# Kernel optimization log

Measured on AMD Instinct MI355X. Metric: run time of the kernel, lower is better.

Reference implementation:

```python
import jax, jax.numpy as jnp
import numpy as np

N_NODES = 50000
N_EDGES = 1000000
IN_DIM, HID_DIM, OUT_DIM = 128, 64, 16


def setup_inputs() -> dict:
    key = jax.random.key(0)
    k1, k2, k3, k4 = jax.random.split(key, 4)
    x = jax.random.normal(k1, (N_NODES, IN_DIM), dtype=jnp.float32)
    edge_index = jax.random.randint(k2, (2, N_EDGES), 0, N_NODES, dtype=jnp.int64)
    # Glorot-style scaling for weights, zero bias (PyG GCNConv default init style)
    W1 = jax.random.normal(k3, (IN_DIM, HID_DIM), dtype=jnp.float32) * (1.0 / np.sqrt(IN_DIM))
    b1 = jnp.zeros((HID_DIM,), dtype=jnp.float32)
    W2 = jax.random.normal(k4, (HID_DIM, OUT_DIM), dtype=jnp.float32) * (1.0 / np.sqrt(HID_DIM))
    b2 = jnp.zeros((OUT_DIM,), dtype=jnp.float32)
    return {"x": x, "edge_index": edge_index, "W1": W1, "b1": b1, "W2": W2, "b2": b2}


def gcn_conv(x, src, dst, W, b, num_nodes):
    """PyG GCNConv: add self loops, symmetric deg^{-1/2} normalization,
    linear transform, gather-scale-scatter aggregation, bias."""
    # degree includes self loops (src/dst already augmented by caller)
    deg = jax.ops.segment_sum(jnp.ones_like(dst, dtype=x.dtype), dst, num_segments=num_nodes)
    dinv = jnp.where(deg > 0, deg ** -0.5, 0.0)
    norm = dinv[src] * dinv[dst]            # [E']
    h = x @ W                                # [N, F_out] transform before aggregation
    msg = h[src] * norm[:, None]             # gather + scale
    out = jax.ops.segment_sum(msg, dst, num_segments=num_nodes)  # scatter-add
    return out + b


def reference(x, edge_index, W1, b1, W2, b2):
    n = x.shape[0]
    loops = jnp.arange(n, dtype=edge_index.dtype)
    src = jnp.concatenate([edge_index[0], loops])
    dst = jnp.concatenate([edge_index[1], loops])
    h = gcn_conv(x, src, dst, W1, b1, n)
    h = jax.nn.relu(h)
    out = gcn_conv(h, src, dst, W2, b2, n)
    return out
```

## Files before the change

### kernel.cpp

```cpp
#include <hip/hip_runtime.h>

#define IN_DIM 128
#define HID_DIM 64
#define OUT_DIM 16

#define SSHIFT 7
#define SMASK 127
#define CHUNK 4096
#define CBLK 256
#define KPT (CHUNK / CBLK)
#define CAP 4096

static __device__ __forceinline__ unsigned short f2bf(float f) {
    unsigned u = __float_as_uint(f);
    unsigned r = u + 0x7fffu + ((u >> 16) & 1u);
    return (unsigned short)(r >> 16);
}
static __device__ __forceinline__ unsigned packbf2(float a, float b) {
    return (unsigned)f2bf(a) | ((unsigned)f2bf(b) << 16);
}
static __device__ __forceinline__ float bflo(unsigned v) { return __uint_as_float(v << 16); }
static __device__ __forceinline__ float bfhi(unsigned v) { return __uint_as_float(v & 0xffff0000u); }

__global__ __launch_bounds__(CBLK) void passC2(const int* __restrict__ src,
                                               const int* __restrict__ dst,
                                               int* __restrict__ gcnt,
                                               int* __restrict__ eb,
                                               int E, int NS) {
    __shared__ int cnt[512];
    __shared__ int bofs[512];
    int t = threadIdx.x;
    for (int s = t; s < NS; s += CBLK) cnt[s] = 0;
    __syncthreads();
    int base = blockIdx.x * CHUNK;
    int dreg[KPT];
    #pragma unroll
    for (int k = 0; k < KPT; ++k) {
        int i = base + k * CBLK + t;
        int d = -1;
        if (i < E) { d = dst[i]; atomicAdd(&cnt[d >> SSHIFT], 1); }
        dreg[k] = d;
    }
    __syncthreads();
    for (int s = t; s < NS; s += CBLK) {
        int c = cnt[s];
        bofs[s] = c ? atomicAdd(&gcnt[s], c) : 0;
        cnt[s] = 0;
    }
    __syncthreads();
    #pragma unroll
    for (int k = 0; k < KPT; ++k) {
        int i = base + k * CBLK + t;
        if (i < E) {
            int d = dreg[k];
            int s = d >> SSHIFT;
            int off = atomicAdd(&cnt[s], 1);
            eb[(size_t)s * CAP + bofs[s] + off] = src[i] | ((d & SMASK) << 17);
        }
    }
}

__global__ __launch_bounds__(256) void passD(const int* __restrict__ eb,
                                             const int* __restrict__ tot,
                                             int* __restrict__ csr_src,
                                             int* __restrict__ row_ptr,
                                             float* __restrict__ dinv,
                                             int N, int E, int NS) {
    __shared__ int red[256];
    __shared__ int deg[128], incl[128], cur[128];
    int s = blockIdx.x, t = threadIdx.x;
    if (t < 128) deg[t] = 0;
    int part = 0;
    for (int k = t; k < s; k += 256) part += tot[k];
    red[t] = part;
    __syncthreads();
    for (int off = 128; off >= 1; off >>= 1) {
        if (t < off) red[t] += red[t + off];
        __syncthreads();
    }
    int b0 = red[0];
    int cnt = tot[s];
    const size_t sbase = (size_t)s * CAP;
    for (int k = t; k < cnt; k += 256) atomicAdd(&deg[eb[sbase + k] >> 17], 1);
    __syncthreads();
    if (t < 128) incl[t] = deg[t];
    __syncthreads();
    for (int off = 1; off < 128; off <<= 1) {
        int tmp = 0;
        if (t < 128 && t >= off) tmp = incl[t - off];
        __syncthreads();
        if (t < 128) incl[t] += tmp;
        __syncthreads();
    }
    if (t < 128) {
        int loff = incl[t] - deg[t];
        cur[t] = b0 + loff;
        int n = (s << SSHIFT) + t;
        if (n < N) {
            row_ptr[n] = b0 + loff;
            dinv[n] = rsqrtf((float)(deg[t] + 1));
        }
    }
    if (s == NS - 1 && t == 0) row_ptr[N] = E;
    __syncthreads();
    for (int k = t; k < cnt; k += 256) {
        int v = eb[sbase + k];
        int dl = v >> 17;
        int p = atomicAdd(&cur[dl], 1);
        csr_src[p] = v & 0x1FFFF;
    }
}

__global__ __launch_bounds__(256) void gemm1_kernel(const float* __restrict__ x,
                                                    const float* __restrict__ W1,
                                                    const float* __restrict__ dinv,
                                                    unsigned* __restrict__ h1u, int N) {
    __shared__ __align__(16) float sW[IN_DIM * HID_DIM];
    __shared__ __align__(16) float sx[16 * IN_DIM];
    int t = threadIdx.x;
    int node0 = blockIdx.x * 16;

    const float4* W4  = (const float4*)W1;
    float4*       sW4 = (float4*)sW;
    for (int i = t; i < (IN_DIM * HID_DIM) / 4; i += 256) sW4[i] = W4[i];

    const float4* x4  = (const float4*)x;
    float4*       sx4 = (float4*)sx;
    for (int i = t; i < (16 * IN_DIM) / 4; i += 256) {
        int r = i >> 5, c = i & 31;
        int n = node0 + r; if (n >= N) n = 0;
        sx4[(r << 5) + c] = x4[(size_t)n * 32 + c];
    }
    __syncthreads();

    int ln = t >> 4, jj = t & 15;
    int n = node0 + ln;
    float4 acc = {0.f, 0.f, 0.f, 0.f};
    const float* xr = sx + ln * IN_DIM;
    #pragma unroll 4
    for (int k = 0; k < IN_DIM; ++k) {
        float  xk = xr[k];
        float4 wv = ((const float4*)(sW + k * HID_DIM))[jj];
        acc.x += xk * wv.x; acc.y += xk * wv.y; acc.z += xk * wv.z; acc.w += xk * wv.w;
    }
    if (n <= N) {
        float dn = (n < N) ? dinv[n] : 0.f;
        uint2 pv;
        pv.x = packbf2(acc.x * dn, acc.y * dn);
        pv.y = packbf2(acc.z * dn, acc.w * dn);
        ((uint2*)(h1u + (size_t)n * 32))[jj] = pv;
    }
}

__global__ __launch_bounds__(256) void agg1_kernel(const unsigned* __restrict__ h1u,
                                                   const int* __restrict__ row_ptr,
                                                   const int* __restrict__ csr_src,
                                                   const float* __restrict__ dinv,
                                                   const float* __restrict__ b1,
                                                   const float* __restrict__ W2,
                                                   unsigned* __restrict__ h2u, int N) {
    __shared__ __align__(16) float sW[OUT_DIM * 68];
    int t = threadIdx.x;
    for (int i = t; i < HID_DIM * OUT_DIM; i += 256) {
        int k = i >> 4, j = i & 15;
        sW[j * 68 + k] = W2[i];
    }
    __syncthreads();

    int lane = t & 63;
    int h  = lane >> 5;
    int l  = lane & 31;
    int es = l >> 3;
    int dg = l & 7;
    int n = blockIdx.x * 8 + ((t >> 6) << 1) + h;
    if (n > N) return;
    if (n == N) {
        if (l < 4) { uint2 z; z.x = 0u; z.y = 0u; ((uint2*)h2u)[(size_t)N * 4 + l] = z; }
        return;
    }

    int e0 = row_ptr[n], e1 = row_ptr[n + 1];
    const uint4* rb = (const uint4*)h1u;
    int sb = h << 5;

    float a0 = 0.f, a1 = 0.f, a2 = 0.f, a3 = 0.f,
          a4 = 0.f, a5 = 0.f, a6 = 0.f, a7 = 0.f;

    for (int base = e0 - 1; base < e1; base += 32) {
        int idx = base + l;
        int sld = N;
        if (idx == e0 - 1) sld = n;
        else if (idx < e1) sld = csr_src[idx];
        int lim = e1 - base;
        if (lim > 32) lim = 32;
        int nr = (lim + 3) >> 2;
        nr = (nr + 1) & ~1;
        for (int r = 0; r < nr; r += 2) {
            int sA = __shfl(sld, sb + ((r + 0) << 2) + es);
            int sB = __shfl(sld, sb + ((r + 1) << 2) + es);
            uint4 vA = rb[(size_t)sA * 8 + dg];
            uint4 vB = rb[(size_t)sB * 8 + dg];
            a0 += bflo(vA.x) + bflo(vB.x);
            a1 += bfhi(vA.x) + bfhi(vB.x);
            a2 += bflo(vA.y) + bflo(vB.y);
            a3 += bfhi(vA.y) + bfhi(vB.y);
            a4 += bflo(vA.z) + bflo(vB.z);
            a5 += bfhi(vA.z) + bfhi(vB.z);
            a6 += bflo(vA.w) + bflo(vB.w);
            a7 += bfhi(vA.w) + bfhi(vB.w);
        }
    }
    #pragma unroll
    for (int m = 8; m <= 16; m <<= 1) {
        a0 += __shfl_xor(a0, m); a1 += __shfl_xor(a1, m);
        a2 += __shfl_xor(a2, m); a3 += __shfl_xor(a3, m);
        a4 += __shfl_xor(a4, m); a5 += __shfl_xor(a5, m);
        a6 += __shfl_xor(a6, m); a7 += __shfl_xor(a7, m);
    }

    float dn = dinv[n];
    float4 bA = ((const float4*)b1)[2 * dg];
    float4 bB = ((const float4*)b1)[2 * dg + 1];
    float r0 = fmaxf(fmaf(dn, a0, bA.x), 0.f);
    float r1 = fmaxf(fmaf(dn, a1, bA.y), 0.f);
    float r2 = fmaxf(fmaf(dn, a2, bA.z), 0.f);
    float r3 = fmaxf(fmaf(dn, a3, bA.w), 0.f);
    float r4 = fmaxf(fmaf(dn, a4, bB.x), 0.f);
    float r5 = fmaxf(fmaf(dn, a5, bB.y), 0.f);
    float r6 = fmaxf(fmaf(dn, a6, bB.z), 0.f);
    float r7 = fmaxf(fmaf(dn, a7, bB.w), 0.f);

    const float* wb = sW + ((es << 2) * 68) + (dg << 3);
    float4 wA, wB2;
    wA = *(const float4*)(wb);        wB2 = *(const float4*)(wb + 4);
    float p0 = r0*wA.x + r1*wA.y + r2*wA.z + r3*wA.w + r4*wB2.x + r5*wB2.y + r6*wB2.z + r7*wB2.w;
    wA = *(const float4*)(wb + 68);   wB2 = *(const float4*)(wb + 72);
    float p1 = r0*wA.x + r1*wA.y + r2*wA.z + r3*wA.w + r4*wB2.x + r5*wB2.y + r6*wB2.z + r7*wB2.w;
    wA = *(const float4*)(wb + 136);  wB2 = *(const float4*)(wb + 140);
    float p2 = r0*wA.x + r1*wA.y + r2*wA.z + r3*wA.w + r4*wB2.x + r5*wB2.y + r6*wB2.z + r7*wB2.w;
    wA = *(const float4*)(wb + 204);  wB2 = *(const float4*)(wb + 208);
    float p3 = r0*wA.x + r1*wA.y + r2*wA.z + r3*wA.w + r4*wB2.x + r5*wB2.y + r6*wB2.z + r7*wB2.w;

    #pragma unroll
    for (int m = 1; m <= 4; m <<= 1) {
        p0 += __shfl_xor(p0, m); p1 += __shfl_xor(p1, m);
        p2 += __shfl_xor(p2, m); p3 += __shfl_xor(p3, m);
    }
    if (dg == 0) {
        uint2 pv;
        pv.x = packbf2(p0 * dn, p1 * dn);
        pv.y = packbf2(p2 * dn, p3 * dn);
        ((uint2*)h2u)[(size_t)n * 4 + es] = pv;
    }
}

__global__ __launch_bounds__(256) void agg2_kernel(const unsigned* __restrict__ h2u,
                                                   const int* __restrict__ row_ptr,
                                                   const int* __restrict__ csr_src,
                                                   const float* __restrict__ dinv,
                                                   const float* __restrict__ b2,
                                                   float* __restrict__ out, int N) {
    int t = threadIdx.x;
    int lane = t & 63;
    int h  = lane >> 4;
    int l  = lane & 15;
    int es = l >> 2;
    int dg = l & 3;
    int n = blockIdx.x * 16 + ((t >> 6) << 2) + h;
    if (n >= N) return;

    int e0 = row_ptr[n], e1 = row_ptr[n + 1];
    const uint2* rb = (const uint2*)h2u;
    int sb = h << 4;

    float a0 = 0.f, a1 = 0.f, a2 = 0.f, a3 = 0.f;

    for (int base = e0 - 1; base < e1; base += 16) {
        int idx = base + l;
        int sld = N;
        if (idx == e0 - 1) sld = n;
        else if (idx < e1) sld = csr_src[idx];
        int lim = e1 - base;
        if (lim > 16) lim = 16;
        int nr = (lim + 3) >> 2;
        nr = (nr + 1) & ~1;
        for (int r = 0; r < nr; r += 2) {
            int sA = __shfl(sld, sb + ((r + 0) << 2) + es);
            int sB = __shfl(sld, sb + ((r + 1) << 2) + es);
            uint2 vA = rb[(size_t)sA * 4 + dg];
            uint2 vB = rb[(size_t)sB * 4 + dg];
            a0 += bflo(vA.x) + bflo(vB.x);
            a1 += bfhi(vA.x) + bfhi(vB.x);
            a2 += bflo(vA.y) + bflo(vB.y);
            a3 += bfhi(vA.y) + bfhi(vB.y);
        }
    }
    #pragma unroll
    for (int m = 4; m <= 8; m <<= 1) {
        a0 += __shfl_xor(a0, m); a1 += __shfl_xor(a1, m);
        a2 += __shfl_xor(a2, m); a3 += __shfl_xor(a3, m);
    }
    if (es == 0) {
        float dn = dinv[n];
        float4 bb = ((const float4*)b2)[dg];
        float4 r;
        r.x = fmaf(dn, a0, bb.x);
        r.y = fmaf(dn, a1, bb.y);
        r.z = fmaf(dn, a2, bb.z);
        r.w = fmaf(dn, a3, bb.w);
        ((float4*)out)[(size_t)n * 4 + dg] = r;
    }
}

extern "C" void kernel_launch(void* const* d_in, const int* in_sizes, int n_in,
                              void* d_out, int out_size, void* d_ws, size_t ws_size,
                              hipStream_t stream) {
    const float* x  = (const float*)d_in[0];
    const int*   ei = (const int*)d_in[1];
    const float* W1 = (const float*)d_in[2];
    const float* b1 = (const float*)d_in[3];
    const float* W2 = (const float*)d_in[4];
    const float* b2 = (const float*)d_in[5];
    float* out = (float*)d_out;

    const int N = in_sizes[0] / IN_DIM;
    const int E = in_sizes[1] / 2;
    const int* src = ei;
    const int* dst = ei + E;

    const int NS  = (N + SMASK) >> SSHIFT;
    const int NSP = NS + 1;
    const int BC  = (E + CHUNK - 1) / CHUNK;

    char* w = (char*)d_ws;
    auto alloc = [&](size_t bytes) -> void* {
        void* p = (void*)w;
        w += (bytes + 255) & ~(size_t)255;
        return p;
    };
    int*      gcnt    = (int*)     alloc((size_t)NSP * 4);
    int*      eb      = (int*)     alloc((size_t)NS * CAP * 4);
    int*      csr_src = (int*)     alloc((size_t)E * 4);
    int*      row_ptr = (int*)     alloc((size_t)(N + 1) * 4);
    float*    dinv    = (float*)   alloc((size_t)N * 4);
    unsigned* h1u     = (unsigned*)alloc((size_t)(N + 1) * 32 * 4);
    unsigned* h2u     = (unsigned*)alloc((size_t)(N + 1) * 8 * 4);

    const int GB  = (N + 16) / 16;
    const int AB1 = (N + 8) / 8;
    const int AB2 = (N + 15) / 16;

    hipMemsetAsync(gcnt, 0, (size_t)NSP * 4, stream);
    passC2<<<BC, CBLK, 0, stream>>>(src, dst, gcnt, eb, E, NS);
    passD <<<NS, 256,  0, stream>>>(eb, gcnt, csr_src, row_ptr, dinv, N, E, NS);

    gemm1_kernel<<<GB, 256, 0, stream>>>(x, W1, dinv, h1u, N);
    agg1_kernel<<<AB1, 256, 0, stream>>>(h1u, row_ptr, csr_src, dinv, b1, W2, h2u, N);
    agg2_kernel<<<AB2, 256, 0, stream>>>(h2u, row_ptr, csr_src, dinv, b2, out, N);
}
```

Before: 165.8 us.

## Fuse edge bucketing with GEMM1 and apply source normalization during aggregation

The bucketing pass and the first dense transform now run as one launch, with block ranges split between the two jobs. This removes the dependency of the GEMM on dinv, so the two can overlap and one launch is saved. The source-side dinv scaling moves into agg1 as an extra per-edge gather of dinv[src] feeding FMAs. The GEMM also reads W1 straight from global memory instead of staging it in shared memory. The risk is the extra per-edge load in agg1, plus cached global reads of W1 in every GEMM block.

```diff
diff --git a/kernel.cpp b/kernel.cpp
--- a/kernel.cpp
+++ b/kernel.cpp
@@ -22,40 +22,81 @@
 static __device__ __forceinline__ float bflo(unsigned v) { return __uint_as_float(v << 16); }
 static __device__ __forceinline__ float bfhi(unsigned v) { return __uint_as_float(v & 0xffff0000u); }
 
-__global__ __launch_bounds__(CBLK) void passC2(const int* __restrict__ src,
-                                               const int* __restrict__ dst,
-                                               int* __restrict__ gcnt,
-                                               int* __restrict__ eb,
-                                               int E, int NS) {
-    __shared__ int cnt[512];
-    __shared__ int bofs[512];
-    int t = threadIdx.x;
-    for (int s = t; s < NS; s += CBLK) cnt[s] = 0;
-    __syncthreads();
-    int base = blockIdx.x * CHUNK;
-    int dreg[KPT];
-    #pragma unroll
-    for (int k = 0; k < KPT; ++k) {
-        int i = base + k * CBLK + t;
-        int d = -1;
-        if (i < E) { d = dst[i]; atomicAdd(&cnt[d >> SSHIFT], 1); }
-        dreg[k] = d;
-    }
-    __syncthreads();
-    for (int s = t; s < NS; s += CBLK) {
-        int c = cnt[s];
-        bofs[s] = c ? atomicAdd(&gcnt[s], c) : 0;
-        cnt[s] = 0;
-    }
-    __syncthreads();
-    #pragma unroll
-    for (int k = 0; k < KPT; ++k) {
-        int i = base + k * CBLK + t;
-        if (i < E) {
-            int d = dreg[k];
-            int s = d >> SSHIFT;
-            int off = atomicAdd(&cnt[s], 1);
-            eb[(size_t)s * CAP + bofs[s] + off] = src[i] | ((d & SMASK) << 17);
+__global__ __launch_bounds__(256) void build_kernel(const float* __restrict__ x,
+                                                    const int* __restrict__ ei,
+                                                    const float* __restrict__ W1,
+                                                    int* __restrict__ gcnt,
+                                                    int* __restrict__ eb,
+                                                    unsigned* __restrict__ h1u,
+                                                    int N, int E, int NS, int BC) {
+    __shared__ __align__(16) int smem[2048];
+    const int t = threadIdx.x;
+    const int b = blockIdx.x;
+
+    if (b < BC) {
+        const int* src = ei;
+        const int* dst = ei + E;
+        int* cnt  = smem;
+        int* bofs = smem + 512;
+        for (int s = t; s < NS; s += CBLK) cnt[s] = 0;
+        __syncthreads();
+        int base = b * CHUNK;
+        int dreg[KPT];
+        #pragma unroll
+        for (int k = 0; k < KPT; ++k) {
+            int i = base + k * CBLK + t;
+            int d = -1;
+            if (i < E) { d = dst[i]; atomicAdd(&cnt[d >> SSHIFT], 1); }
+            dreg[k] = d;
+        }
+        __syncthreads();
+        for (int s = t; s < NS; s += CBLK) {
+            int c = cnt[s];
+            bofs[s] = c ? atomicAdd(&gcnt[s], c) : 0;
+            cnt[s] = 0;
+        }
+        __syncthreads();
+        #pragma unroll
+        for (int k = 0; k < KPT; ++k) {
+            int i = base + k * CBLK + t;
+            if (i < E) {
+                int d = dreg[k];
+                int s = d >> SSHIFT;
+                int off = atomicAdd(&cnt[s], 1);
+                eb[(size_t)s * CAP + bofs[s] + off] = src[i] | ((d & SMASK) << 17);
+            }
+        }
+    } else {
+        float* sx = (float*)smem;
+        int node0 = (b - BC) * 16;
+        const float4* x4  = (const float4*)x;
+        float4*       sx4 = (float4*)sx;
+        for (int i = t; i < 512; i += 256) {
+            int r = i >> 5, c = i & 31;
+            int n = node0 + r; if (n >= N) n = 0;
+            sx4[(r << 5) + c] = x4[(size_t)n * 32 + c];
+        }
+        __syncthreads();
+        int ln = t >> 4, jj = t & 15;
+        int n = node0 + ln;
+        const float4* W4 = (const float4*)W1;
+        float4 acc = {0.f, 0.f, 0.f, 0.f};
+        const float* xr = sx + ln * IN_DIM;
+        #pragma unroll 4
+        for (int k = 0; k < IN_DIM; ++k) {
+            float  xk = xr[k];
+            float4 wv = W4[k * 16 + jj];
+            acc.x += xk * wv.x; acc.y += xk * wv.y;
+            acc.z += xk * wv.z; acc.w += xk * wv.w;
+        }
+        if (n < N) {
+            uint2 pv;
+            pv.x = packbf2(acc.x, acc.y);
+            pv.y = packbf2(acc.z, acc.w);
+            ((uint2*)(h1u + (size_t)n * 32))[jj] = pv;
+        } else if (n == N) {
+            uint2 z; z.x = 0u; z.y = 0u;
+            ((uint2*)(h1u + (size_t)N * 32))[jj] = z;
         }
     }
 }
@@ -101,54 +142,13 @@
             dinv[n] = rsqrtf((float)(deg[t] + 1));
         }
     }
-    if (s == NS - 1 && t == 0) row_ptr[N] = E;
+    if (s == NS - 1 && t == 0) { row_ptr[N] = E; dinv[N] = 0.f; }
     __syncthreads();
     for (int k = t; k < cnt; k += 256) {
         int v = eb[sbase + k];
         int dl = v >> 17;
         int p = atomicAdd(&cur[dl], 1);
         csr_src[p] = v & 0x1FFFF;
-    }
-}
-
-__global__ __launch_bounds__(256) void gemm1_kernel(const float* __restrict__ x,
-                                                    const float* __restrict__ W1,
-                                                    const float* __restrict__ dinv,
-                                                    unsigned* __restrict__ h1u, int N) {
-    __shared__ __align__(16) float sW[IN_DIM * HID_DIM];
-    __shared__ __align__(16) float sx[16 * IN_DIM];
-    int t = threadIdx.x;
-    int node0 = blockIdx.x * 16;
-
-    const float4* W4  = (const float4*)W1;
-    float4*       sW4 = (float4*)sW;
-    for (int i = t; i < (IN_DIM * HID_DIM) / 4; i += 256) sW4[i] = W4[i];
-
-    const float4* x4  = (const float4*)x;
-    float4*       sx4 = (float4*)sx;
-    for (int i = t; i < (16 * IN_DIM) / 4; i += 256) {
-        int r = i >> 5, c = i & 31;
-        int n = node0 + r; if (n >= N) n = 0;
-        sx4[(r << 5) + c] = x4[(size_t)n * 32 + c];
-    }
-    __syncthreads();
-
-    int ln = t >> 4, jj = t & 15;
-    int n = node0 + ln;
-    float4 acc = {0.f, 0.f, 0.f, 0.f};
-    const float* xr = sx + ln * IN_DIM;
-    #pragma unroll 4
-    for (int k = 0; k < IN_DIM; ++k) {
-        float  xk = xr[k];
-        float4 wv = ((const float4*)(sW + k * HID_DIM))[jj];
-        acc.x += xk * wv.x; acc.y += xk * wv.y; acc.z += xk * wv.z; acc.w += xk * wv.w;
-    }
-    if (n <= N) {
-        float dn = (n < N) ? dinv[n] : 0.f;
-        uint2 pv;
-        pv.x = packbf2(acc.x * dn, acc.y * dn);
-        pv.y = packbf2(acc.z * dn, acc.w * dn);
-        ((uint2*)(h1u + (size_t)n * 32))[jj] = pv;
     }
 }
 
@@ -200,14 +200,16 @@
             int sB = __shfl(sld, sb + ((r + 1) << 2) + es);
             uint4 vA = rb[(size_t)sA * 8 + dg];
             uint4 vB = rb[(size_t)sB * 8 + dg];
-            a0 += bflo(vA.x) + bflo(vB.x);
-            a1 += bfhi(vA.x) + bfhi(vB.x);
-            a2 += bflo(vA.y) + bflo(vB.y);
-            a3 += bfhi(vA.y) + bfhi(vB.y);
-            a4 += bflo(vA.z) + bflo(vB.z);
-            a5 += bfhi(vA.z) + bfhi(vB.z);
-            a6 += bflo(vA.w) + bflo(vB.w);
-            a7 += bfhi(vA.w) + bfhi(vB.w);
+            float wA = dinv[sA];
+            float wB = dinv[sB];
+            a0 = fmaf(wA, bflo(vA.x), fmaf(wB, bflo(vB.x), a0));
+            a1 = fmaf(wA, bfhi(vA.x), fmaf(wB, bfhi(vB.x), a1));
+            a2 = fmaf(wA, bflo(vA.y), fmaf(wB, bflo(vB.y), a2));
+            a3 = fmaf(wA, bfhi(vA.y), fmaf(wB, bfhi(vB.y), a3));
+            a4 = fmaf(wA, bflo(vA.z), fmaf(wB, bflo(vB.z), a4));
+            a5 = fmaf(wA, bfhi(vA.z), fmaf(wB, bfhi(vB.z), a5));
+            a6 = fmaf(wA, bflo(vA.w), fmaf(wB, bflo(vB.w), a6));
+            a7 = fmaf(wA, bfhi(vA.w), fmaf(wB, bfhi(vB.w), a7));
         }
     }
     #pragma unroll
@@ -325,12 +327,10 @@
 
     const int N = in_sizes[0] / IN_DIM;
     const int E = in_sizes[1] / 2;
-    const int* src = ei;
-    const int* dst = ei + E;
-
     const int NS  = (N + SMASK) >> SSHIFT;
     const int NSP = NS + 1;
     const int BC  = (E + CHUNK - 1) / CHUNK;
+    const int GB  = (N + 16) / 16;
 
     char* w = (char*)d_ws;
     auto alloc = [&](size_t bytes) -> void* {
@@ -342,19 +342,16 @@
     int*      eb      = (int*)     alloc((size_t)NS * CAP * 4);
     int*      csr_src = (int*)     alloc((size_t)E * 4);
     int*      row_ptr = (int*)     alloc((size_t)(N + 1) * 4);
-    float*    dinv    = (float*)   alloc((size_t)N * 4);
+    float*    dinv    = (float*)   alloc((size_t)(N + 1) * 4);
     unsigned* h1u     = (unsigned*)alloc((size_t)(N + 1) * 32 * 4);
     unsigned* h2u     = (unsigned*)alloc((size_t)(N + 1) * 8 * 4);
 
-    const int GB  = (N + 16) / 16;
     const int AB1 = (N + 8) / 8;
     const int AB2 = (N + 15) / 16;
 
     hipMemsetAsync(gcnt, 0, (size_t)NSP * 4, stream);
-    passC2<<<BC, CBLK, 0, stream>>>(src, dst, gcnt, eb, E, NS);
+    build_kernel<<<BC + GB, 256, 0, stream>>>(x, ei, W1, gcnt, eb, h1u, N, E, NS, BC);
     passD <<<NS, 256,  0, stream>>>(eb, gcnt, csr_src, row_ptr, dinv, N, E, NS);
-
-    gemm1_kernel<<<GB, 256, 0, stream>>>(x, W1, dinv, h1u, N);
     agg1_kernel<<<AB1, 256, 0, stream>>>(h1u, row_ptr, csr_src, dinv, b1, W2, h2u, N);
     agg2_kernel<<<AB2, 256, 0, stream>>>(h2u, row_ptr, csr_src, dinv, b2, out, N);
 }
```

After: 181.6 us. 1.09x slower.

## Register-tile gemm1 over 4 nodes per thread with 64-node blocks

Applied to the files above, without the earlier changes.

The first-layer GEMM now processes 64 nodes per block, and each thread computes a 4x4 output tile instead of a 1x4 one. Each W1 float4 read from shared memory is reused across four nodes, and the 32 KB W1 copy into LDS is amortized over four times as many nodes. The x tile is padded to a stride of 132 to reduce bank conflicts. The costs are more registers and larger LDS use per block (about 66 KB), which lowers the number of resident blocks, and a grid roughly four times smaller.

```diff
diff --git a/kernel.cpp b/kernel.cpp
--- a/kernel.cpp
+++ b/kernel.cpp
@@ -10,6 +10,9 @@
 #define CBLK 256
 #define KPT (CHUNK / CBLK)
 #define CAP 4096
+
+#define G1N 64
+#define G1S 132
 
 static __device__ __forceinline__ unsigned short f2bf(float f) {
     unsigned u = __float_as_uint(f);
@@ -116,40 +119,61 @@
                                                     const float* __restrict__ dinv,
                                                     unsigned* __restrict__ h1u, int N) {
     __shared__ __align__(16) float sW[IN_DIM * HID_DIM];
-    __shared__ __align__(16) float sx[16 * IN_DIM];
+    __shared__ __align__(16) float sx[G1N * G1S];
     int t = threadIdx.x;
-    int node0 = blockIdx.x * 16;
+    int node0 = blockIdx.x * G1N;
 
     const float4* W4  = (const float4*)W1;
     float4*       sW4 = (float4*)sW;
-    for (int i = t; i < (IN_DIM * HID_DIM) / 4; i += 256) sW4[i] = W4[i];
-
-    const float4* x4  = (const float4*)x;
-    float4*       sx4 = (float4*)sx;
-    for (int i = t; i < (16 * IN_DIM) / 4; i += 256) {
+    #pragma unroll
+    for (int i = 0; i < 8; ++i) sW4[i * 256 + t] = W4[i * 256 + t];
+
+    const float4* x4 = (const float4*)x;
+    for (int i = t; i < G1N * 32; i += 256) {
         int r = i >> 5, c = i & 31;
         int n = node0 + r; if (n >= N) n = 0;
-        sx4[(r << 5) + c] = x4[(size_t)n * 32 + c];
-    }
-    __syncthreads();
-
-    int ln = t >> 4, jj = t & 15;
-    int n = node0 + ln;
-    float4 acc = {0.f, 0.f, 0.f, 0.f};
-    const float* xr = sx + ln * IN_DIM;
+        *(float4*)(sx + r * G1S + c * 4) = x4[(size_t)n * 32 + c];
+    }
+    __syncthreads();
+
+    int og = t & 15, ng = t >> 4;
+    float a00=0.f,a01=0.f,a02=0.f,a03=0.f, a10=0.f,a11=0.f,a12=0.f,a13=0.f,
+          a20=0.f,a21=0.f,a22=0.f,a23=0.f, a30=0.f,a31=0.f,a32=0.f,a33=0.f;
+    const float* xr = sx + (ng << 2) * G1S;
     #pragma unroll 4
     for (int k = 0; k < IN_DIM; ++k) {
-        float  xk = xr[k];
-        float4 wv = ((const float4*)(sW + k * HID_DIM))[jj];
-        acc.x += xk * wv.x; acc.y += xk * wv.y; acc.z += xk * wv.z; acc.w += xk * wv.w;
-    }
-    if (n <= N) {
-        float dn = (n < N) ? dinv[n] : 0.f;
-        uint2 pv;
-        pv.x = packbf2(acc.x * dn, acc.y * dn);
-        pv.y = packbf2(acc.z * dn, acc.w * dn);
-        ((uint2*)(h1u + (size_t)n * 32))[jj] = pv;
-    }
+        float x0 = xr[k];
+        float x1 = xr[G1S + k];
+        float x2 = xr[2 * G1S + k];
+        float x3 = xr[3 * G1S + k];
+        float4 wv = ((const float4*)(sW + k * HID_DIM))[og];
+        a00 = fmaf(x0, wv.x, a00); a01 = fmaf(x0, wv.y, a01);
+        a02 = fmaf(x0, wv.z, a02); a03 = fmaf(x0, wv.w, a03);
+        a10 = fmaf(x1, wv.x, a10); a11 = fmaf(x1, wv.y, a11);
+        a12 = fmaf(x1, wv.z, a12); a13 = fmaf(x1, wv.w, a13);
+        a20 = fmaf(x2, wv.x, a20); a21 = fmaf(x2, wv.y, a21);
+        a22 = fmaf(x2, wv.z, a22); a23 = fmaf(x2, wv.w, a23);
+        a30 = fmaf(x3, wv.x, a30); a31 = fmaf(x3, wv.y, a31);
+        a32 = fmaf(x3, wv.z, a32); a33 = fmaf(x3, wv.w, a33);
+    }
+
+    int nb = node0 + (ng << 2);
+#define G1_STORE(i, c0, c1, c2, c3)                                         \
+    {                                                                       \
+        int n = nb + i;                                                     \
+        if (n <= N) {                                                       \
+            float dn = (n < N) ? dinv[n] : 0.f;         \
+            uint2 pv;                                                       \
+            pv.x = packbf2(c0 * dn, c1 * dn);                               \
+            pv.y = packbf2(c2 * dn, c3 * dn);                               \
+            ((uint2*)(h1u + (size_t)n * 32))[og] = pv;                      \
+        }                                                                   \
+    }
+    G1_STORE(0, a00, a01, a02, a03)
+    G1_STORE(1, a10, a11, a12, a13)
+    G1_STORE(2, a20, a21, a22, a23)
+    G1_STORE(3, a30, a31, a32, a33)
+#undef G1_STORE
 }
 
 __global__ __launch_bounds__(256) void agg1_kernel(const unsigned* __restrict__ h1u,
@@ -346,7 +370,7 @@
     unsigned* h1u     = (unsigned*)alloc((size_t)(N + 1) * 32 * 4);
     unsigned* h2u     = (unsigned*)alloc((size_t)(N + 1) * 8 * 4);
 
-    const int GB  = (N + 16) / 16;
+    const int GB  = (N + G1N) / G1N;
     const int AB1 = (N + 8) / 8;
     const int AB2 = (N + 15) / 16;
 
```

Result: no change. 163.2 us (-1.6%).
